# Kernel optimization log

Measured on AMD Instinct MI355X. Metric: run time of the kernel, lower is better.

## Reference

```python
import jax, jax.numpy as jnp
import numpy as np

# ---- DiTAC constants (from init_kwargs) ----
NC = 10          # tess (number of cells on [0,1])
A_LO = -0.5      # a: lower edge of active range
B_HI = 2.0       # b: upper edge of active range
INV_SQRT2 = 0.7071067811865476


def make_basis(nc):
    """Null-space basis B ([2*nc, nc-1]) of the CPA constraint matrix
    (velocity continuity at internal knots + zero boundary), via QR
    of L^T with mode='complete' ('qr' basis in difw).
    Per-cell velocity v_c(x) = a_c*x + b_c, Avees layout [a0,b0,a1,b1,...]."""
    L = np.zeros((nc + 1, 2 * nc))
    for i in range(1, nc):                      # continuity at x_i = i/nc
        xi = i / nc
        L[i - 1, 2 * (i - 1)] = xi
        L[i - 1, 2 * (i - 1) + 1] = 1.0
        L[i - 1, 2 * i] = -xi
        L[i - 1, 2 * i + 1] = -1.0
    L[nc - 1, 1] = 1.0                          # v(0) = 0  ->  b_0 = 0
    L[nc, 2 * (nc - 1)] = 1.0                   # v(1) = 0  ->  a_{nc-1}+b_{nc-1}=0
    L[nc, 2 * (nc - 1) + 1] = 1.0
    q, _ = np.linalg.qr(L.T, mode='complete')
    return q[:, nc + 1:]                        # [2*nc, nc-1]

_B_NP = make_basis(NC)


def cpab_transform(xn, A, nc):
    """Closed-form integration of the piecewise-affine ODE dx/dt = a_c x + b_c
    for t=1, vectorized over all elements. Fixed nc+1 iterations: each
    iteration either finishes (flow stays inside current cell) or advances
    the point to the next cell boundary and deducts the transit time.
    Once finished, t=0 makes psi == x, a stable fixed point."""
    h = 1.0 / nc
    eps = 1e-12
    c = jnp.clip(jnp.floor(xn * nc).astype(jnp.int32), 0, nc - 1)
    t = jnp.ones_like(xn)
    x = xn
    for _ in range(nc + 1):
        a = A[c, 0]
        b = A[c, 1]
        v = a * x + b
        big_a = jnp.abs(a) > 1e-8
        a_safe = jnp.where(big_a, a, 1.0)
        ea = jnp.exp(t * a)
        psi = jnp.where(big_a, ea * x + (b / a_safe) * (ea - 1.0), x + t * b)
        left = c.astype(x.dtype) * h
        right = left + h
        inside = (psi >= left) & (psi <= right)
        xb = jnp.where(v >= 0, right, left)          # boundary being approached
        vb = a * xb + b
        v_safe = jnp.where(jnp.abs(v) > eps, v, jnp.where(v >= 0, eps, -eps))
        t_aff = jnp.log(jnp.maximum(vb / v_safe, eps)) / a_safe
        b_safe = jnp.where(jnp.abs(b) > eps, b, eps)
        t_hit = jnp.where(big_a, t_aff, (xb - x) / b_safe)
        x = jnp.where(inside, psi, xb)
        t = jnp.where(inside, 0.0, jnp.maximum(t - t_hit, 0.0))
        step = jnp.where(v >= 0, 1, -1)
        c = jnp.where(inside, c, jnp.clip(c + step, 0, nc - 1))
    return x


def setup_inputs() -> dict:
    key = jax.random.key(0)
    k1, k2 = jax.random.split(key)
    x = jax.random.normal(k1, (4096, 2048), dtype=jnp.float32)
    thetas = jax.random.normal(k2, (1, NC - 1), dtype=jnp.float32)
    return {"x": x, "thetas": thetas}


def reference(x, thetas):
    B = jnp.asarray(_B_NP, dtype=x.dtype)                 # [2*nc, nc-1]
    A = (B @ thetas[0]).reshape(NC, 2)                    # per-cell (a, b)
    flat = x.reshape(-1)
    mask = (flat >= A_LO) & (flat <= B_HI)
    masked = jnp.where(mask, flat, 0.0)
    xn = (masked - A_LO) / (B_HI - A_LO)                  # norm to [0,1]
    xt = cpab_transform(xn, A, NC)
    data_t = xt * (B_HI - A_LO) + A_LO                    # denorm to [a,b]
    cpab_out = jnp.where(mask, data_t, flat)
    phi = 0.5 * (1.0 + jax.lax.erf(flat * INV_SQRT2))     # Gaussian CDF gate
    return (cpab_out * phi).reshape(x.shape)
```

## Files before the change

kernel.cpp:

```cpp
#include <hip/hip_runtime.h>
#include <math.h>
#include <string.h>

#define NCELLS 10
#define A_LO  -0.5f
#define B_HI   2.0f

#define TBL_LO    -6.5f
#define TBL_HI     6.5f
#define TBL_SCALE  256.0f
#define TBL_BIAS   1664.0f
#define TBL_N      3329
#define TBL_N_PAD  3332

struct BMat { float v[2 * NCELLS][NCELLS - 1]; };

static void compute_B_host(BMat* out) {
    const int m = 2 * NCELLS;
    const int n = NCELLS + 1;
    double A[2 * NCELLS][NCELLS + 1];
    memset(A, 0, sizeof(A));
    for (int i = 1; i < NCELLS; ++i) {
        double xi = (double)i / NCELLS;
        A[2 * (i - 1)][i - 1]     = xi;
        A[2 * (i - 1) + 1][i - 1] = 1.0;
        A[2 * i][i - 1]           = -xi;
        A[2 * i + 1][i - 1]       = -1.0;
    }
    A[1][NCELLS - 1] = 1.0;
    A[2 * (NCELLS - 1)][NCELLS] = 1.0;
    A[2 * (NCELLS - 1) + 1][NCELLS] = 1.0;

    double V[NCELLS + 1][2 * NCELLS];
    double tau[NCELLS + 1];
    for (int j = 0; j < n; ++j) {
        double alpha = A[j][j];
        double xnorm2 = 0.0;
        for (int i = j + 1; i < m; ++i) xnorm2 += A[i][j] * A[i][j];
        for (int i = 0; i < m; ++i) V[j][i] = 0.0;
        V[j][j] = 1.0;
        if (xnorm2 == 0.0) { tau[j] = 0.0; continue; }
        double beta = -copysign(sqrt(alpha * alpha + xnorm2), alpha);
        tau[j] = (beta - alpha) / beta;
        double scale = 1.0 / (alpha - beta);
        for (int i = j + 1; i < m; ++i) V[j][i] = A[i][j] * scale;
        A[j][j] = beta;
        for (int i = j + 1; i < m; ++i) A[i][j] = 0.0;
        for (int k = j + 1; k < n; ++k) {
            double dot = 0.0;
            for (int i = j; i < m; ++i) dot += V[j][i] * A[i][k];
            dot *= tau[j];
            for (int i = j; i < m; ++i) A[i][k] -= V[j][i] * dot;
        }
    }
    for (int c = 0; c < NCELLS - 1; ++c) {
        double q[2 * NCELLS];
        for (int i = 0; i < m; ++i) q[i] = 0.0;
        q[n + c] = 1.0;
        for (int j = n - 1; j >= 0; --j) {
            double dot = 0.0;
            for (int i = j; i < m; ++i) dot += V[j][i] * q[i];
            dot *= tau[j];
            for (int i = j; i < m; ++i) q[i] -= V[j][i] * dot;
        }
        for (int i = 0; i < m; ++i) out->v[i][c] = (float)q[i];
    }
}

__device__ __forceinline__ float eval_node(float f, const float* As) {
    bool mask = (f >= A_LO) && (f <= B_HI);
    float cpab_out = f;
    if (mask) {
        float xn = (f - A_LO) * 0.4f;
        float xx = xn;
        int c = min(max((int)floorf(xn * (float)NCELLS), 0), NCELLS - 1);
        float t = 1.0f;
        #pragma unroll 1
        for (int it = 0; it < NCELLS + 1; ++it) {
            float a = As[2 * c];
            float b = As[2 * c + 1];
            float v = fmaf(a, xx, b);
            bool big_a = fabsf(a) > 1e-8f;
            float a_safe = big_a ? a : 1.0f;
            float ea = __expf(t * a);
            float psi = big_a ? fmaf(ea, xx, (b / a_safe) * (ea - 1.0f))
                              : fmaf(t, b, xx);
            float left  = (float)c * 0.1f;
            float right = left + 0.1f;
            bool inside = (psi >= left) && (psi <= right);
            if (inside) { xx = psi; break; }
            float xb = (v >= 0.f) ? right : left;
            float vb = fmaf(a, xb, b);
            float t_hit;
            if (big_a) {
                float v_safe = (fabsf(v) > 1e-12f) ? v : ((v >= 0.f) ? 1e-12f : -1e-12f);
                t_hit = __logf(fmaxf(vb / v_safe, 1e-12f)) / a_safe;
            } else {
                float b_safe = (fabsf(b) > 1e-12f) ? b : 1e-12f;
                t_hit = (xb - xx) / b_safe;
            }
            xx = xb;
            t = fmaxf(t - t_hit, 0.f);
            c = min(max(c + ((v >= 0.f) ? 1 : -1), 0), NCELLS - 1);
        }
        cpab_out = fmaf(xx, 2.5f, A_LO);
    }
    float phi = 0.5f * (1.0f + erff(f * 0.7071067811865476f));
    return cpab_out * phi;
}

__global__ __launch_bounds__(256) void ditac_fused(
        const float4* __restrict__ x, float4* __restrict__ out,
        const float* __restrict__ theta, BMat B) {
    __shared__ float As[2 * NCELLS];
    __shared__ float T[TBL_N_PAD];
    const int tid = threadIdx.x;
    const int base = blockIdx.x * 2048 + tid;

    float4 vv[8];
    #pragma unroll
    for (int k = 0; k < 8; ++k) vv[k] = x[base + k * 256];

    if (tid < 2 * NCELLS) {
        float s = 0.f;
        #pragma unroll
        for (int k = 0; k < NCELLS - 1; ++k) s += B.v[tid][k] * theta[k];
        As[tid] = s;
    }
    __syncthreads();

    #pragma unroll 1
    for (int j = tid; j < TBL_N; j += 256) {
        float f = TBL_LO + (float)j * (1.0f / TBL_SCALE);
        T[j] = eval_node(f, As);
    }
    __syncthreads();

    #pragma unroll
    for (int k = 0; k < 8; ++k) {
        float in[4] = {vv[k].x, vv[k].y, vv[k].z, vv[k].w};
        float r[4];
        #pragma unroll
        for (int e = 0; e < 4; ++e) {
            float f = in[e];
            float u = fmaf(f, TBL_SCALE, TBL_BIAS);
            float uc = fminf(fmaxf(u, 0.0f), (float)(TBL_N - 1));
            int i = min((int)uc, TBL_N - 2);
            float frac = uc - (float)i;
            float lo = T[i];
            float hi = T[i + 1];
            float val = fmaf(frac, hi - lo, lo);
            r[e] = (f > TBL_HI) ? f : val;
        }
        out[base + k * 256] = make_float4(r[0], r[1], r[2], r[3]);
    }
}

extern "C" void kernel_launch(void* const* d_in, const int* in_sizes, int n_in,
                              void* d_out, int out_size, void* d_ws, size_t ws_size,
                              hipStream_t stream) {
    const float* x     = (const float*)d_in[0];
    const float* theta = (const float*)d_in[1];
    float* out = (float*)d_out;

    BMat B;
    compute_B_host(&B);

    ditac_fused<<<1024, 256, 0, stream>>>(
        (const float4*)x, (float4*)out, theta, B);
}
```

Measured before the change: 22.13 us.

## Use two-resolution lookup table and halve per-block work with more blocks

After: 27.98 us. +26.4%, slower.

```diff
diff --git a/kernel.cpp b/kernel.cpp
--- a/kernel.cpp
+++ b/kernel.cpp
@@ -6,12 +6,12 @@
 #define A_LO  -0.5f
 #define B_HI   2.0f
 
-#define TBL_LO    -6.5f
-#define TBL_HI     6.5f
-#define TBL_SCALE  256.0f
-#define TBL_BIAS   1664.0f
-#define TBL_N      3329
-#define TBL_N_PAD  3332
+#define FINE_OFF   0
+#define FINE_LAST  639.9995f
+#define COARSE_OFF 642
+#define COARSE_LAST 831.9995f
+#define TBL_TOT    1476
+#define F_HI       6.5f
 
 struct BMat { float v[2 * NCELLS][NCELLS - 1]; };
 
@@ -113,13 +113,13 @@
         const float4* __restrict__ x, float4* __restrict__ out,
         const float* __restrict__ theta, BMat B) {
     __shared__ float As[2 * NCELLS];
-    __shared__ float T[TBL_N_PAD];
+    __shared__ float T[TBL_TOT];
     const int tid = threadIdx.x;
-    const int base = blockIdx.x * 2048 + tid;
+    const int base = blockIdx.x * 1024 + tid;
 
-    float4 vv[8];
+    float4 vv[4];
     #pragma unroll
-    for (int k = 0; k < 8; ++k) vv[k] = x[base + k * 256];
+    for (int k = 0; k < 4; ++k) vv[k] = x[base + k * 256];
 
     if (tid < 2 * NCELLS) {
         float s = 0.f;
@@ -130,27 +130,32 @@
     __syncthreads();
 
     #pragma unroll 1
-    for (int j = tid; j < TBL_N; j += 256) {
-        float f = TBL_LO + (float)j * (1.0f / TBL_SCALE);
+    for (int j = tid; j < TBL_TOT; j += 256) {
+        float f;
+        if (j < COARSE_OFF) f = -0.5f + (float)min(j, 640) * (1.0f / 256.0f);
+        else                f = -6.5f + (float)min(j - COARSE_OFF, 832) * (1.0f / 64.0f);
         T[j] = eval_node(f, As);
     }
     __syncthreads();
 
     #pragma unroll
-    for (int k = 0; k < 8; ++k) {
+    for (int k = 0; k < 4; ++k) {
         float in[4] = {vv[k].x, vv[k].y, vv[k].z, vv[k].w};
         float r[4];
         #pragma unroll
         for (int e = 0; e < 4; ++e) {
             float f = in[e];
-            float u = fmaf(f, TBL_SCALE, TBL_BIAS);
-            float uc = fminf(fmaxf(u, 0.0f), (float)(TBL_N - 1));
-            int i = min((int)uc, TBL_N - 2);
-            float frac = uc - (float)i;
+            bool act = (f >= A_LO) && (f <= B_HI);
+            float u    = act ? fmaf(f, 256.f, 128.f) : fmaf(f, 64.f, 416.f);
+            float umax = act ? FINE_LAST : COARSE_LAST;
+            float uc = fminf(fmaxf(u, 0.0f), umax);
+            int il = (int)uc;
+            float frac = uc - (float)il;
+            int i = il + (act ? FINE_OFF : COARSE_OFF);
             float lo = T[i];
             float hi = T[i + 1];
             float val = fmaf(frac, hi - lo, lo);
-            r[e] = (f > TBL_HI) ? f : val;
+            r[e] = (f > F_HI) ? f : val;
         }
         out[base + k * 256] = make_float4(r[0], r[1], r[2], r[3]);
     }
@@ -166,6 +171,6 @@
     BMat B;
     compute_B_host(&B);
 
-    ditac_fused<<<1024, 256, 0, stream>>>(
+    ditac_fused<<<2048, 256, 0, stream>>>(
         (const float4*)x, (float4*)out, theta, B);
 }
```
